# Kernel optimization log

Hardware: AMD Instinct MI355X
Metric: run time of the kernel (lower is better)

The kernel has to match this reference:

```python
import jax, jax.numpy as jnp
import numpy as np

TOP_K = 2  # num_experts_per_tok

def setup_inputs() -> dict:
    key = jax.random.key(0)
    ks = jax.random.split(key, 6)
    B, S, D, E, H = 4, 2048, 1024, 8, 4096
    x  = jax.random.normal(ks[0], (B, S, D), dtype=jnp.float32)
    Wg = jax.random.normal(ks[1], (D, E), dtype=jnp.float32) * 0.02
    W1 = jax.random.normal(ks[2], (E, D, H), dtype=jnp.float32) * 0.02
    b1 = jnp.zeros((E, H), dtype=jnp.float32)
    W2 = jax.random.normal(ks[3], (E, H, D), dtype=jnp.float32) * 0.02
    b2 = jnp.zeros((E, D), dtype=jnp.float32)
    return {"x": x, "Wg": Wg, "W1": W1, "b1": b1, "W2": W2, "b2": b2}

def reference(x, Wg, W1, b1, W2, b2):
    B, S, D = x.shape
    E = Wg.shape[1]
    xf = x.reshape(-1, D)                       # [T, D]
    T = xf.shape[0]
    logits = xf @ Wg                            # [T, E]
    probs = jax.nn.softmax(logits, axis=-1)
    weights, indices = jax.lax.top_k(probs, TOP_K)   # [T, K]
    # Dense combine weights: cw[t, e] = routing weight if e in top-k of t else 0.
    cw = jnp.zeros((T, E), dtype=x.dtype).at[jnp.arange(T)[:, None], indices].set(weights)
    out = jnp.zeros_like(xf)
    for e in range(E):  # small fixed expert count; per-expert GEMMs
        h = jax.nn.gelu(xf @ W1[e] + b1[e], approximate=False)  # [T, H]
        y = h @ W2[e] + b2[e]                                   # [T, D]
        out = out + y * cw[:, e:e + 1]
    return out.reshape(B, S, D)
```

## Files before the change

### kernel.cpp

```cpp
#include <hip/hip_runtime.h>
#include <hip/hip_bf16.h>
#include <stdint.h>

#define D_DIM 1024
#define E_NUM 8
#define H_DIM 4096

typedef __attribute__((ext_vector_type(8))) short short8;
typedef __attribute__((ext_vector_type(4))) short short4v;
typedef __attribute__((ext_vector_type(4))) unsigned short ushort4v;
typedef __attribute__((ext_vector_type(4))) float f32x4;

#define GLOBAL_AS __attribute__((address_space(1)))
#define LDS_AS __attribute__((address_space(3)))

__device__ __forceinline__ void async_load16(const void* g, void* l) {
    __builtin_amdgcn_global_load_lds((GLOBAL_AS void*)g, (LDS_AS void*)l, 16, 0, 0);
}

__device__ __forceinline__ float gelu_fast(float x) {
    float x3 = x * x * x;
    float z = 0.7978845608028654f * x + 0.0356774081363001f * x3;
    float u = __expf(-2.0f * fabsf(z));
    float t = __fdividef(1.0f - u, 1.0f + u);
    t = copysignf(t, z);
    return 0.5f * x * (1.0f + t);
}

__device__ __forceinline__ float b2f(short s) {
    union { float f; unsigned u; } x; x.u = ((unsigned)(unsigned short)s) << 16; return x.f;
}

__device__ __forceinline__ unsigned short f2b(float f) {
    union { __hip_bfloat16 h; unsigned short s; } u;
    u.h = __float2bfloat16(f);
    return u.s;
}

__global__ __launch_bounds__(256) void router_kernel(
    const float* __restrict__ x, const float* __restrict__ Wg,
    __hip_bfloat16* __restrict__ xb, int* __restrict__ epick,
    float* __restrict__ ewgt, int T) {
    int gwave = (int)((blockIdx.x * 256 + threadIdx.x) >> 6);
    int lane = threadIdx.x & 63;
    if (gwave >= T) return;
    const float* xr = x + (size_t)gwave * D_DIM;
    double acc[E_NUM];
#pragma unroll
    for (int e = 0; e < E_NUM; ++e) acc[e] = 0.0;
#pragma unroll
    for (int i = 0; i < D_DIM / 64; ++i) {
        int d = i * 64 + lane;
        float xv = xr[d];
        xb[(size_t)gwave * D_DIM + d] = __float2bfloat16(xv);
        const float4* wgp = (const float4*)(Wg + (size_t)d * E_NUM);
        float4 wa = wgp[0], wb = wgp[1];
        double xd = (double)xv;
        acc[0] += xd * (double)wa.x; acc[1] += xd * (double)wa.y;
        acc[2] += xd * (double)wa.z; acc[3] += xd * (double)wa.w;
        acc[4] += xd * (double)wb.x; acc[5] += xd * (double)wb.y;
        acc[6] += xd * (double)wb.z; acc[7] += xd * (double)wb.w;
    }
#pragma unroll
    for (int s = 32; s > 0; s >>= 1) {
#pragma unroll
        for (int e = 0; e < E_NUM; ++e) acc[e] += __shfl_xor(acc[e], s);
    }
    double mx = acc[0];
#pragma unroll
    for (int e = 1; e < E_NUM; ++e) mx = fmax(mx, acc[e]);
    double p[E_NUM]; double sum = 0.0;
#pragma unroll
    for (int e = 0; e < E_NUM; ++e) { p[e] = exp(acc[e] - mx); sum += p[e]; }
    int i0 = 0;
#pragma unroll
    for (int e = 1; e < E_NUM; ++e) if (p[e] > p[i0]) i0 = e;
    int i1 = (i0 == 0) ? 1 : 0;
#pragma unroll
    for (int e = 0; e < E_NUM; ++e) if (e != i0 && p[e] > p[i1]) i1 = e;
    if (lane == 0) {
        epick[gwave] = i0 | (i1 << 8);
        ewgt[2 * gwave]     = (float)(p[i0] / sum);
        ewgt[2 * gwave + 1] = (float)(p[i1] / sum);
    }
}

__global__ __launch_bounds__(256) void bucket_kernel(
    const int* __restrict__ epick, int* __restrict__ cnt,
    int* __restrict__ tok, int* __restrict__ eidx, int T) {
    __shared__ int lcnt[E_NUM];
    __shared__ int gbase[E_NUM];
    int b = blockIdx.x, tid = threadIdx.x;
    if (tid < E_NUM) lcnt[tid] = 0;
    __syncthreads();
    int t = b * 128 + (tid >> 1);
    int j = tid & 1;
    int e = (epick[t] >> (j * 8)) & 0xff;
    int li = atomicAdd(&lcnt[e], 1);
    __syncthreads();
    if (tid < E_NUM) gbase[tid] = atomicAdd(&cnt[tid], lcnt[tid]);
    __syncthreads();
    int slot = gbase[e] + li;
    tok[e * T + slot] = t;
    eidx[2 * t + j] = (e << 16) | slot;
}

__global__ void prefix_kernel(const int* __restrict__ cnt, int* __restrict__ base) {
    if (threadIdx.x == 0) {
        int a = 0;
#pragma unroll
        for (int e = 0; e < E_NUM; ++e) { base[e] = a; a += cnt[e]; }
    }
}

__global__ __launch_bounds__(256) void transpose_both_kernel(
    const float* __restrict__ W1, const float* __restrict__ W2,
    __hip_bfloat16* __restrict__ w1t, __hip_bfloat16* __restrict__ w2t) {
    __shared__ float tile[64][65];
    int e = blockIdx.z;
    int id = blockIdx.x;
    const float* src; unsigned short* dst; int R, C, r0, c0, perm;
    if (id < 1024) {
        R = D_DIM; C = H_DIM;
        r0 = (id >> 6) * 64; c0 = (id & 63) * 64;
        src = W1 + (size_t)e * D_DIM * H_DIM;
        dst = (unsigned short*)(w1t + (size_t)e * H_DIM * D_DIM);
        perm = 0;
    } else {
        id -= 1024;
        R = H_DIM; C = D_DIM;
        r0 = (id >> 4) * 64; c0 = (id & 15) * 64;
        src = W2 + (size_t)e * H_DIM * D_DIM;
        dst = (unsigned short*)(w2t + (size_t)e * D_DIM * H_DIM);
        perm = 1;
    }
    int tx = threadIdx.x, ty = threadIdx.y;
#pragma unroll
    for (int i = 0; i < 8; ++i) {
        int j = ty + i * 8;
        int sr = perm ? ((j & 3) * 16 + (j >> 2)) : j;
        float2 v = *(const float2*)(src + (size_t)(r0 + sr) * C + c0 + 2 * tx);
        tile[j][2 * tx] = v.x; tile[j][2 * tx + 1] = v.y;
    }
    __syncthreads();
#pragma unroll
    for (int i = 0; i < 8; ++i) {
        int cc = ty + i * 8;
        unsigned pk = (unsigned)f2b(tile[2 * tx][cc]) | ((unsigned)f2b(tile[2 * tx + 1][cc]) << 16);
        *(unsigned*)(dst + (size_t)(c0 + cc) * R + r0 + 2 * tx) = pk;
    }
}


__global__ __launch_bounds__(512) void gemm1_kernel(
    const __hip_bfloat16* __restrict__ xb,
    const __hip_bfloat16* __restrict__ w1t,
    const float* __restrict__ b1,
    const int* __restrict__ cnt, const int* __restrict__ base,
    const int* __restrict__ tok,
    __hip_bfloat16* __restrict__ hbuf,
    int T) {
    int e = blockIdx.z;
    int M = cnt[e];
    int m0 = blockIdx.y * 256;
    if (m0 >= M) return;
    int n0 = blockIdx.x * 256;
    const __hip_bfloat16* Bp = w1t + (size_t)e * H_DIM * D_DIM;

    __shared__ __align__(16) short sA[4][256 * 32];
    __shared__ __align__(16) short sB[4][256 * 32];
    __shared__ float sBias[256];

    int tid = threadIdx.x;
    int w = tid >> 6, lane = tid & 63;
    int wm = w >> 2, wn = w & 3;
    int q = lane >> 4, l4 = lane & 15;

    if (tid < 256) sBias[tid] = b1[e * H_DIM + n0 + tid];

    int kswz = ((lane & 3) ^ ((lane >> 3) & 3)) << 3;
    int r0 = w * 32 + (lane >> 2);
    int r1 = r0 + 16;
    int tA0 = tok[e * T + min(m0 + r0, M - 1)];
    int tA1 = tok[e * T + min(m0 + r1, M - 1)];
    const __hip_bfloat16* gA0 = xb + (size_t)tA0 * D_DIM + kswz;
    const __hip_bfloat16* gA1 = xb + (size_t)tA1 * D_DIM + kswz;
    const __hip_bfloat16* gB0 = Bp + (size_t)(n0 + r0) * D_DIM + kswz;
    const __hip_bfloat16* gB1 = Bp + (size_t)(n0 + r1) * D_DIM + kswz;

    f32x4 acc[8][4];
#pragma unroll
    for (int a = 0; a < 8; ++a)
#pragma unroll
        for (int b = 0; b < 4; ++b) acc[a][b] = (f32x4){0.f, 0.f, 0.f, 0.f};

    auto stage = [&](int tt) {
        int bi = tt & 3, kk = tt * 32;
        char* la = (char*)sA[bi] + w * 2048;
        char* lb = (char*)sB[bi] + w * 2048;
        async_load16(gA0 + kk, la);
        async_load16(gA1 + kk, la + 1024);
        async_load16(gB0 + kk, lb);
        async_load16(gB1 + kk, lb + 1024);
    };
    auto body = [&](int tt) {
        const char* pa = (const char*)sA[tt & 3];
        const char* pb = (const char*)sB[tt & 3];
        short8 bF[4];
#pragma unroll
        for (int n = 0; n < 4; ++n) {
            int rb = wn * 64 + n * 16 + l4;
            bF[n] = *(const short8*)(pb + rb * 64 + ((q ^ ((rb >> 1) & 3)) << 4));
        }
        __builtin_amdgcn_s_setprio(1);
#pragma unroll
        for (int m = 0; m < 8; ++m) {
            int ra = wm * 128 + m * 16 + l4;
            short8 aF = *(const short8*)(pa + ra * 64 + ((q ^ ((ra >> 1) & 3)) << 4));
#pragma unroll
            for (int n = 0; n < 4; ++n)
                acc[m][n] = __builtin_amdgcn_mfma_f32_16x16x32_bf16(aF, bF[n], acc[m][n], 0, 0, 0);
        }
        __builtin_amdgcn_s_setprio(0);
    };

    const int nt = D_DIM / 32;
    asm volatile("s_waitcnt vmcnt(0)" ::: "memory");
    stage(0); stage(1); stage(2);
    asm volatile("s_waitcnt vmcnt(8)" ::: "memory");
    __builtin_amdgcn_s_barrier();
    for (int t = 0; t < nt - 3; ++t) {
        stage(t + 3);
        body(t);
        asm volatile("s_waitcnt vmcnt(8)" ::: "memory");
        __builtin_amdgcn_s_barrier();
    }
    body(nt - 3);
    asm volatile("s_waitcnt vmcnt(4)" ::: "memory");
    __builtin_amdgcn_s_barrier();
    body(nt - 2);
    asm volatile("s_waitcnt vmcnt(0)" ::: "memory");
    __builtin_amdgcn_s_barrier();
    body(nt - 1);

    int sb = base[e];
    unsigned short* hs = (unsigned short*)hbuf;
#pragma unroll
    for (int m = 0; m < 8; ++m) {
        int rbase = wm * 128 + m * 16 + q * 4;
#pragma unroll
        for (int i = 0; i < 4; ++i) {
            int row = m0 + rbase + i;
            if (row < M) {
                size_t hrow = (size_t)(sb + row) * H_DIM;
                ushort4v pk;
#pragma unroll
                for (int n = 0; n < 4; ++n) {
                    float v = acc[m][n][i] + sBias[wn * 64 + n * 16 + l4];
                    pk[n] = f2b(gelu_fast(v));
                }
                *(ushort4v*)(hs + hrow + n0 + wn * 64 + l4 * 4) = pk;
            }
        }
    }
}

__global__ __launch_bounds__(512) void gemm2_kernel(
    const __hip_bfloat16* __restrict__ hbuf,
    const __hip_bfloat16* __restrict__ w2t,
    const int* __restrict__ cnt, const int* __restrict__ base,
    __hip_bfloat16* __restrict__ ybuf,
    int T) {
    int e = blockIdx.z >> 1;
    int kc = blockIdx.z & 1;
    int M = cnt[e];
    int m0 = blockIdx.y * 256;
    if (m0 >= M) return;
    int n0 = blockIdx.x * 256;
    int sb = base[e];
    const __hip_bfloat16* Bp = w2t + (size_t)e * D_DIM * H_DIM;

    __shared__ __align__(16) short sA[4][256 * 32];
    __shared__ __align__(16) short sB[4][256 * 32];

    int tid = threadIdx.x;
    int w = tid >> 6, lane = tid & 63;
    int wm = w >> 2, wn = w & 3;
    int q = lane >> 4, l4 = lane & 15;

    int kswz = ((lane & 3) ^ ((lane >> 3) & 3)) << 3;
    int r0 = w * 32 + (lane >> 2);
    int r1 = r0 + 16;
    int k0 = kc * (H_DIM / 2);
    const __hip_bfloat16* gA0 = hbuf + (size_t)(sb + min(m0 + r0, M - 1)) * H_DIM + k0 + kswz;
    const __hip_bfloat16* gA1 = hbuf + (size_t)(sb + min(m0 + r1, M - 1)) * H_DIM + k0 + kswz;
    const __hip_bfloat16* gB0 = Bp + (size_t)(n0 + r0) * H_DIM + k0 + kswz;
    const __hip_bfloat16* gB1 = Bp + (size_t)(n0 + r1) * H_DIM + k0 + kswz;

    f32x4 acc[8][4];
#pragma unroll
    for (int a = 0; a < 8; ++a)
#pragma unroll
        for (int b = 0; b < 4; ++b) acc[a][b] = (f32x4){0.f, 0.f, 0.f, 0.f};

    auto stage = [&](int tt) {
        int bi = tt & 3, kk = tt * 32;
        char* la = (char*)sA[bi] + w * 2048;
        char* lb = (char*)sB[bi] + w * 2048;
        async_load16(gA0 + kk, la);
        async_load16(gA1 + kk, la + 1024);
        async_load16(gB0 + kk, lb);
        async_load16(gB1 + kk, lb + 1024);
    };
    auto body = [&](int tt) {
        const char* pa = (const char*)sA[tt & 3];
        const char* pb = (const char*)sB[tt & 3];
        short8 bF[4];
#pragma unroll
        for (int n = 0; n < 4; ++n) {
            int rb = wn * 64 + n * 16 + l4;
            bF[n] = *(const short8*)(pb + rb * 64 + ((q ^ ((rb >> 1) & 3)) << 4));
        }
        __builtin_amdgcn_s_setprio(1);
#pragma unroll
        for (int m = 0; m < 8; ++m) {
            int ra = wm * 128 + m * 16 + l4;
            short8 aF = *(const short8*)(pa + ra * 64 + ((q ^ ((ra >> 1) & 3)) << 4));
#pragma unroll
            for (int n = 0; n < 4; ++n)
                acc[m][n] = __builtin_amdgcn_mfma_f32_16x16x32_bf16(aF, bF[n], acc[m][n], 0, 0, 0);
        }
        __builtin_amdgcn_s_setprio(0);
    };

    const int nt = (H_DIM / 2) / 32;
    asm volatile("s_waitcnt vmcnt(0)" ::: "memory");
    stage(0); stage(1); stage(2);
    asm volatile("s_waitcnt vmcnt(8)" ::: "memory");
    __builtin_amdgcn_s_barrier();
    for (int t = 0; t < nt - 3; ++t) {
        stage(t + 3);
        body(t);
        asm volatile("s_waitcnt vmcnt(8)" ::: "memory");
        __builtin_amdgcn_s_barrier();
    }
    body(nt - 3);
    asm volatile("s_waitcnt vmcnt(4)" ::: "memory");
    __builtin_amdgcn_s_barrier();
    body(nt - 2);
    asm volatile("s_waitcnt vmcnt(0)" ::: "memory");
    __builtin_amdgcn_s_barrier();
    body(nt - 1);

    size_t ybase = (size_t)kc * 2 * T;
    unsigned short* ys = (unsigned short*)ybuf;
#pragma unroll
    for (int m = 0; m < 8; ++m) {
        int rbase = wm * 128 + m * 16 + q * 4;
#pragma unroll
        for (int i = 0; i < 4; ++i) {
            int row = m0 + rbase + i;
            if (row < M) {
                size_t yrow = (ybase + sb + row) * D_DIM;
                ushort4v pk;
#pragma unroll
                for (int n = 0; n < 4; ++n) pk[n] = f2b(acc[m][n][i]);
                *(ushort4v*)(ys + yrow + n0 + wn * 64 + l4 * 4) = pk;
            }
        }
    }
}

__global__ __launch_bounds__(256) void combine_kernel(
    const __hip_bfloat16* __restrict__ yb, const float* __restrict__ b2,
    const int* __restrict__ base, const int* __restrict__ eidx,
    const float* __restrict__ ewgt, float* __restrict__ out, int T) {
    int t = blockIdx.x, tid = threadIdx.x;
    int v0 = eidx[2 * t], v1 = eidx[2 * t + 1];
    float w0 = ewgt[2 * t], w1 = ewgt[2 * t + 1];
    int e0 = v0 >> 16, e1 = v1 >> 16;
    size_t g0 = (size_t)base[e0] + (v0 & 0xffff);
    size_t g1 = (size_t)base[e1] + (v1 & 0xffff);
    int c = tid * 4;
    int blk = c >> 6;
    int tt = (c >> 2) & 15;
    size_t off2 = (size_t)2 * T * D_DIM;
    const short* ys = (const short*)yb;
    short4v a0 = *(const short4v*)(ys + g0 * D_DIM + c);
    short4v a1 = *(const short4v*)(ys + off2 + g0 * D_DIM + c);
    short4v c0 = *(const short4v*)(ys + g1 * D_DIM + c);
    short4v c1 = *(const short4v*)(ys + off2 + g1 * D_DIM + c);
    float s0[4] = { b2f(a0.x) + b2f(a1.x), b2f(a0.y) + b2f(a1.y),
                    b2f(a0.z) + b2f(a1.z), b2f(a0.w) + b2f(a1.w) };
    float s1[4] = { b2f(c0.x) + b2f(c1.x), b2f(c0.y) + b2f(c1.y),
                    b2f(c0.z) + b2f(c1.z), b2f(c0.w) + b2f(c1.w) };
    float* orow = out + (size_t)t * D_DIM;
#pragma unroll
    for (int s = 0; s < 4; ++s) {
        int oc = blk * 64 + s * 16 + tt;
        float o = w0 * (s0[s] + b2[(size_t)e0 * D_DIM + oc]) +
                  w1 * (s1[s] + b2[(size_t)e1 * D_DIM + oc]);
        orow[oc] = o;
    }
}

extern "C" void kernel_launch(void* const* d_in, const int* in_sizes, int n_in,
                              void* d_out, int out_size, void* d_ws, size_t ws_size,
                              hipStream_t stream) {
    const float* x  = (const float*)d_in[0];
    const float* Wg = (const float*)d_in[1];
    const float* W1 = (const float*)d_in[2];
    const float* b1 = (const float*)d_in[3];
    const float* W2 = (const float*)d_in[4];
    const float* b2 = (const float*)d_in[5];
    int T = in_sizes[0] / D_DIM;

    char* p = (char*)d_ws;
    int* cnt   = (int*)p;
    int* base  = (int*)(p + 256);
    int* tok   = (int*)(p + 512);
    int* eidx  = (int*)(p + 512 + 4ll * E_NUM * T);
    float* ewgt = (float*)(p + 512 + 4ll * E_NUM * T + 8ll * T);
    int* epick = (int*)(p + 512 + 4ll * E_NUM * T + 16ll * T);
    char* pb = p + 512 + 4ll * E_NUM * T + 20ll * T;
    __hip_bfloat16* xb  = (__hip_bfloat16*)pb;
    __hip_bfloat16* w1t = xb + (size_t)T * D_DIM;
    __hip_bfloat16* w2t = w1t + (size_t)E_NUM * H_DIM * D_DIM;
    __hip_bfloat16* hb  = w2t + (size_t)E_NUM * H_DIM * D_DIM;
    __hip_bfloat16* yb  = xb;

    hipMemsetAsync(cnt, 0, 256, stream);

    router_kernel<<<dim3((T + 3) / 4), 256, 0, stream>>>(x, Wg, xb, epick, ewgt, T);
    bucket_kernel<<<dim3(T / 128), 256, 0, stream>>>(epick, cnt, tok, eidx, T);
    prefix_kernel<<<1, 64, 0, stream>>>(cnt, base);
    transpose_both_kernel<<<dim3(2048, 1, E_NUM), dim3(32, 8), 0, stream>>>(W1, W2, w1t, w2t);
    gemm1_kernel<<<dim3(H_DIM / 256, T / 256, E_NUM), 512, 0, stream>>>(xb, w1t, b1, cnt, base, tok, hb, T);
    gemm2_kernel<<<dim3(D_DIM / 256, T / 256, E_NUM * 2), 512, 0, stream>>>(hb, w2t, cnt, base, yb, T);
    combine_kernel<<<T, 256, 0, stream>>>(yb, b2, base, eidx, ewgt, (float*)d_out, T);
}
```

Baseline: 882.2 us.

## Split MFMA tile into two barrier-separated phases interleaved with staged async loads

Restructures the main loop of both GEMM kernels into a ping-pong style schedule. Each k-tile is split into two half-MFMA phases separated by workgroup barriers, and the A and B async global-to-LDS loads are issued between the phases. LDS fragment offsets are precomputed and the loop is unrolled by four so buffer indices become constants. The goal is better overlap of LDS reads, global loads and MFMA work across waves, at the cost of more barriers per tile and a fragile vmcnt accounting.

```diff
diff --git a/kernel.cpp b/kernel.cpp
--- a/kernel.cpp
+++ b/kernel.cpp
@@ -152,6 +152,52 @@
 }
 
 
+#define MOE_TILE(BI, KK, DO_STAGE, VM)                                         \
+    {                                                                          \
+        const char* pa_ = (const char*)sA + (BI) * 16384;                      \
+        const char* pb_ = (const char*)sB + (BI) * 16384;                      \
+        short8 aF[4], bF[4];                                                   \
+        _Pragma("unroll")                                                      \
+        for (int n = 0; n < 4; ++n) bF[n] = *(const short8*)(pb_ + offB[n]);   \
+        _Pragma("unroll")                                                      \
+        for (int m = 0; m < 4; ++m) aF[m] = *(const short8*)(pa_ + offA[m]);   \
+        if (DO_STAGE) {                                                        \
+            char* dA_ = stA + (((BI) + 3) & 3) * 16384;                        \
+            async_load16(gA0 + (KK), dA_);                                     \
+            async_load16(gA1 + (KK), dA_ + 1024);                              \
+        }                                                                      \
+        __builtin_amdgcn_s_barrier();                                          \
+        __builtin_amdgcn_s_setprio(1);                                         \
+        _Pragma("unroll")                                                      \
+        for (int m = 0; m < 4; ++m)                                            \
+            _Pragma("unroll")                                                  \
+            for (int n = 0; n < 4; ++n)                                        \
+                acc[m][n] = __builtin_amdgcn_mfma_f32_16x16x32_bf16(           \
+                    aF[m], bF[n], acc[m][n], 0, 0, 0);                         \
+        __builtin_amdgcn_s_setprio(0);                                         \
+        __builtin_amdgcn_s_barrier();                                          \
+        _Pragma("unroll")                                                      \
+        for (int m = 0; m < 4; ++m) aF[m] = *(const short8*)(pa_ + offA[4 + m]); \
+        if (DO_STAGE) {                                                        \
+            char* dB_ = stB + (((BI) + 3) & 3) * 16384;                        \
+            async_load16(gB0 + (KK), dB_);                                     \
+            async_load16(gB1 + (KK), dB_ + 1024);                              \
+        }                                                                      \
+        if ((VM) == 8) asm volatile("s_waitcnt vmcnt(8)" ::: "memory");        \
+        else if ((VM) == 4) asm volatile("s_waitcnt vmcnt(4)" ::: "memory");   \
+        else if ((VM) == 0) asm volatile("s_waitcnt vmcnt(0)" ::: "memory");   \
+        __builtin_amdgcn_s_barrier();                                          \
+        __builtin_amdgcn_s_setprio(1);                                         \
+        _Pragma("unroll")                                                      \
+        for (int m = 0; m < 4; ++m)                                            \
+            _Pragma("unroll")                                                  \
+            for (int n = 0; n < 4; ++n)                                        \
+                acc[4 + m][n] = __builtin_amdgcn_mfma_f32_16x16x32_bf16(       \
+                    aF[m], bF[n], acc[4 + m][n], 0, 0, 0);                     \
+        __builtin_amdgcn_s_setprio(0);                                         \
+        __builtin_amdgcn_s_barrier();                                          \
+    }
+
 __global__ __launch_bounds__(512) void gemm1_kernel(
     const __hip_bfloat16* __restrict__ xb,
     const __hip_bfloat16* __restrict__ w1t,
@@ -187,6 +233,20 @@
     const __hip_bfloat16* gA1 = xb + (size_t)tA1 * D_DIM + kswz;
     const __hip_bfloat16* gB0 = Bp + (size_t)(n0 + r0) * D_DIM + kswz;
     const __hip_bfloat16* gB1 = Bp + (size_t)(n0 + r1) * D_DIM + kswz;
+    char* stA = (char*)sA + w * 2048;
+    char* stB = (char*)sB + w * 2048;
+
+    int offA[8], offB[4];
+#pragma unroll
+    for (int m = 0; m < 8; ++m) {
+        int ra = wm * 128 + m * 16 + l4;
+        offA[m] = ra * 64 + ((q ^ ((ra >> 1) & 3)) << 4);
+    }
+#pragma unroll
+    for (int n = 0; n < 4; ++n) {
+        int rb = wn * 64 + n * 16 + l4;
+        offB[n] = rb * 64 + ((q ^ ((rb >> 1) & 3)) << 4);
+    }
 
     f32x4 acc[8][4];
 #pragma unroll
@@ -195,53 +255,31 @@
         for (int b = 0; b < 4; ++b) acc[a][b] = (f32x4){0.f, 0.f, 0.f, 0.f};
 
     auto stage = [&](int tt) {
-        int bi = tt & 3, kk = tt * 32;
-        char* la = (char*)sA[bi] + w * 2048;
-        char* lb = (char*)sB[bi] + w * 2048;
+        int kk = tt * 32;
+        char* la = stA + (tt & 3) * 16384;
+        char* lb = stB + (tt & 3) * 16384;
         async_load16(gA0 + kk, la);
         async_load16(gA1 + kk, la + 1024);
         async_load16(gB0 + kk, lb);
         async_load16(gB1 + kk, lb + 1024);
     };
-    auto body = [&](int tt) {
-        const char* pa = (const char*)sA[tt & 3];
-        const char* pb = (const char*)sB[tt & 3];
-        short8 bF[4];
-#pragma unroll
-        for (int n = 0; n < 4; ++n) {
-            int rb = wn * 64 + n * 16 + l4;
-            bF[n] = *(const short8*)(pb + rb * 64 + ((q ^ ((rb >> 1) & 3)) << 4));
-        }
-        __builtin_amdgcn_s_setprio(1);
-#pragma unroll
-        for (int m = 0; m < 8; ++m) {
-            int ra = wm * 128 + m * 16 + l4;
-            short8 aF = *(const short8*)(pa + ra * 64 + ((q ^ ((ra >> 1) & 3)) << 4));
-#pragma unroll
-            for (int n = 0; n < 4; ++n)
-                acc[m][n] = __builtin_amdgcn_mfma_f32_16x16x32_bf16(aF, bF[n], acc[m][n], 0, 0, 0);
-        }
-        __builtin_amdgcn_s_setprio(0);
-    };
 
     const int nt = D_DIM / 32;
     asm volatile("s_waitcnt vmcnt(0)" ::: "memory");
     stage(0); stage(1); stage(2);
     asm volatile("s_waitcnt vmcnt(8)" ::: "memory");
     __builtin_amdgcn_s_barrier();
-    for (int t = 0; t < nt - 3; ++t) {
-        stage(t + 3);
-        body(t);
-        asm volatile("s_waitcnt vmcnt(8)" ::: "memory");
-        __builtin_amdgcn_s_barrier();
-    }
-    body(nt - 3);
-    asm volatile("s_waitcnt vmcnt(4)" ::: "memory");
-    __builtin_amdgcn_s_barrier();
-    body(nt - 2);
-    asm volatile("s_waitcnt vmcnt(0)" ::: "memory");
-    __builtin_amdgcn_s_barrier();
-    body(nt - 1);
+    MOE_TILE(0, 3 * 32, 1, 8);
+    for (int i = 0; i < (nt - 4) / 4; ++i) {
+        int tb = 1 + i * 4;
+        MOE_TILE(1, (tb + 3) * 32, 1, 8);
+        MOE_TILE(2, (tb + 4) * 32, 1, 8);
+        MOE_TILE(3, (tb + 5) * 32, 1, 8);
+        MOE_TILE(0, (tb + 6) * 32, 1, 8);
+    }
+    MOE_TILE(1, 0, 0, 4);
+    MOE_TILE(2, 0, 0, 0);
+    MOE_TILE(3, 0, 0, -1);
 
     int sb = base[e];
     unsigned short* hs = (unsigned short*)hbuf;
@@ -296,6 +334,20 @@
     const __hip_bfloat16* gA1 = hbuf + (size_t)(sb + min(m0 + r1, M - 1)) * H_DIM + k0 + kswz;
     const __hip_bfloat16* gB0 = Bp + (size_t)(n0 + r0) * H_DIM + k0 + kswz;
     const __hip_bfloat16* gB1 = Bp + (size_t)(n0 + r1) * H_DIM + k0 + kswz;
+    char* stA = (char*)sA + w * 2048;
+    char* stB = (char*)sB + w * 2048;
+
+    int offA[8], offB[4];
+#pragma unroll
+    for (int m = 0; m < 8; ++m) {
+        int ra = wm * 128 + m * 16 + l4;
+        offA[m] = ra * 64 + ((q ^ ((ra >> 1) & 3)) << 4);
+    }
+#pragma unroll
+    for (int n = 0; n < 4; ++n) {
+        int rb = wn * 64 + n * 16 + l4;
+        offB[n] = rb * 64 + ((q ^ ((rb >> 1) & 3)) << 4);
+    }
 
     f32x4 acc[8][4];
 #pragma unroll
@@ -304,53 +356,31 @@
         for (int b = 0; b < 4; ++b) acc[a][b] = (f32x4){0.f, 0.f, 0.f, 0.f};
 
     auto stage = [&](int tt) {
-        int bi = tt & 3, kk = tt * 32;
-        char* la = (char*)sA[bi] + w * 2048;
-        char* lb = (char*)sB[bi] + w * 2048;
+        int kk = tt * 32;
+        char* la = stA + (tt & 3) * 16384;
+        char* lb = stB + (tt & 3) * 16384;
         async_load16(gA0 + kk, la);
         async_load16(gA1 + kk, la + 1024);
         async_load16(gB0 + kk, lb);
         async_load16(gB1 + kk, lb + 1024);
     };
-    auto body = [&](int tt) {
-        const char* pa = (const char*)sA[tt & 3];
-        const char* pb = (const char*)sB[tt & 3];
-        short8 bF[4];
-#pragma unroll
-        for (int n = 0; n < 4; ++n) {
-            int rb = wn * 64 + n * 16 + l4;
-            bF[n] = *(const short8*)(pb + rb * 64 + ((q ^ ((rb >> 1) & 3)) << 4));
-        }
-        __builtin_amdgcn_s_setprio(1);
-#pragma unroll
-        for (int m = 0; m < 8; ++m) {
-            int ra = wm * 128 + m * 16 + l4;
-            short8 aF = *(const short8*)(pa + ra * 64 + ((q ^ ((ra >> 1) & 3)) << 4));
-#pragma unroll
-            for (int n = 0; n < 4; ++n)
-                acc[m][n] = __builtin_amdgcn_mfma_f32_16x16x32_bf16(aF, bF[n], acc[m][n], 0, 0, 0);
-        }
-        __builtin_amdgcn_s_setprio(0);
-    };
 
     const int nt = (H_DIM / 2) / 32;
     asm volatile("s_waitcnt vmcnt(0)" ::: "memory");
     stage(0); stage(1); stage(2);
     asm volatile("s_waitcnt vmcnt(8)" ::: "memory");
     __builtin_amdgcn_s_barrier();
-    for (int t = 0; t < nt - 3; ++t) {
-        stage(t + 3);
-        body(t);
-        asm volatile("s_waitcnt vmcnt(8)" ::: "memory");
-        __builtin_amdgcn_s_barrier();
-    }
-    body(nt - 3);
-    asm volatile("s_waitcnt vmcnt(4)" ::: "memory");
-    __builtin_amdgcn_s_barrier();
-    body(nt - 2);
-    asm volatile("s_waitcnt vmcnt(0)" ::: "memory");
-    __builtin_amdgcn_s_barrier();
-    body(nt - 1);
+    MOE_TILE(0, 3 * 32, 1, 8);
+    for (int i = 0; i < (nt - 4) / 4; ++i) {
+        int tb = 1 + i * 4;
+        MOE_TILE(1, (tb + 3) * 32, 1, 8);
+        MOE_TILE(2, (tb + 4) * 32, 1, 8);
+        MOE_TILE(3, (tb + 5) * 32, 1, 8);
+        MOE_TILE(0, (tb + 6) * 32, 1, 8);
+    }
+    MOE_TILE(1, 0, 0, 4);
+    MOE_TILE(2, 0, 0, 0);
+    MOE_TILE(3, 0, 0, -1);
 
     size_t ybase = (size_t)kc * 2 * T;
     unsigned short* ys = (unsigned short*)ybuf;
```

Result: faster. 787.5 us (-10.7%).
